# Performance work log

Hardware: AMD Instinct MI355X
Metric: run time of the kernel (lower is better)

## Reference

```python
import jax, jax.numpy as jnp
import numpy as np

B, T, D, H = 16, 2048, 1024, 64  # batch, seq_len(block_sz), emb_dim, head_sz


def setup_inputs() -> dict:
    key = jax.random.key(0)
    k0, k1, k2, k3 = jax.random.split(key, 4)
    x = jax.random.normal(k0, (B, T, D), dtype=jnp.float32)
    # nn.Linear(D, H, bias=False) weights, stored as [D, H] so y = x @ W
    s = 1.0 / np.sqrt(D)
    Wq = jax.random.uniform(k1, (D, H), dtype=jnp.float32, minval=-s, maxval=s)
    Wk = jax.random.uniform(k2, (D, H), dtype=jnp.float32, minval=-s, maxval=s)
    Wv = jax.random.uniform(k3, (D, H), dtype=jnp.float32, minval=-s, maxval=s)
    return {"x": x, "Wq": Wq, "Wk": Wk, "Wv": Wv}


def reference(x, Wq, Wk, Wv):
    # Single-head causal self-attention, naive (materializes full [B,T,T] scores).
    q = x @ Wq  # [B, T, H]
    k = x @ Wk  # [B, T, H]
    v = x @ Wv  # [B, T, H]
    scale = 1.0 / (q.shape[-1] ** 0.5)
    w = jnp.einsum("btd,bsd->bts", q, k) * scale  # [B, T, T]
    causal = jnp.tril(jnp.ones((T, T), dtype=bool))
    w = jnp.where(causal, w, -jnp.inf)
    w = jax.nn.softmax(w, axis=-1)
    # dropout p=0.0 -> identity
    out = jnp.einsum("bts,bsd->btd", w, v)  # [B, T, H]
    return out
```

## Files before the change

### kernel.cpp

```cpp
#include <hip/hip_runtime.h>
#include <hip/hip_bf16.h>
#include <math.h>

#define BB 16
#define TT 2048
#define DD 1024
#define HH 64
#define QK_SCALE 0.18033688011112042f

typedef short bf16x8 __attribute__((ext_vector_type(8)));
typedef short bf16x4 __attribute__((ext_vector_type(4)));
typedef float f32x4 __attribute__((ext_vector_type(4)));

__device__ __forceinline__ short f2bf(float f) {
  union { float f; unsigned u; } c; c.f = f;
  unsigned u = c.u + 0x7FFFu + ((c.u >> 16) & 1u);
  return (short)(u >> 16);
}

__device__ __forceinline__ unsigned pk2(float lo, float hi) {
  float2 t; t.x = lo; t.y = hi;
  __hip_bfloat162 h = __float22bfloat162_rn(t);
  union { __hip_bfloat162 h; unsigned u; } c; c.h = h;
  return c.u;
}

#define FENCE_VM(N)                                        \
  do {                                                     \
    asm volatile("s_waitcnt vmcnt(" #N ")" ::: "memory");  \
    __builtin_amdgcn_sched_barrier(0);                     \
    __builtin_amdgcn_s_barrier();                          \
  } while (0)

__device__ __forceinline__ void* lds_swz(void* base, int row, int col) {
  int byte = (row << 7) + (col << 1);
  byte ^= (row & 7) << 4;
  return (void*)((char*)base + byte);
}

__global__ __launch_bounds__(256) void pack_wt(
    const float* __restrict__ Wq, const float* __restrict__ Wk,
    const float* __restrict__ Wv, short* __restrict__ wt) {
  const int idx = blockIdx.x * 256 + threadIdx.x;
  const int n = idx >> 7;
  const int k0 = (idx & 127) << 3;
  const float* W = (n < 64) ? Wq : (n < 128) ? Wk : Wv;
  const int h = n & 63;
  bf16x8 o;
#pragma unroll
  for (int j = 0; j < 8; ++j) o[j] = f2bf(W[(k0 + j) * HH + h]);
  *(bf16x8*)&wt[n * DD + k0] = o;
}

__global__ __launch_bounds__(256, 2) void qkv_mfma(
    const float* __restrict__ x, const short* __restrict__ wt,
    short* __restrict__ qo, short* __restrict__ ko, short* __restrict__ vt) {
  __shared__ float xls[4][64 * 64];
  const int tid = threadIdx.x;
  const int lane = tid & 63;
  const int w = tid >> 6;
  const int q16 = lane & 15;
  const int g = lane >> 4;
  const size_t r0 = (size_t)blockIdx.x * 64;

  f32x4 acc[4][3];
#pragma unroll
  for (int mf = 0; mf < 4; ++mf)
#pragma unroll
    for (int nf = 0; nf < 3; ++nf) acc[mf][nf] = (f32x4){0.f, 0.f, 0.f, 0.f};

  const short* wp[3];
#pragma unroll
  for (int nf = 0; nf < 3; ++nf)
    wp[nf] = wt + (size_t)(w * 48 + nf * 16 + q16) * DD + g * 8;

  const int srow_b = w * 16 + (lane >> 4);
  const int ul = lane & 15;

  bf16x8 bcur[3][2];
#pragma unroll
  for (int nf = 0; nf < 3; ++nf)
#pragma unroll
    for (int kf = 0; kf < 2; ++kf)
      bcur[nf][kf] = *(const bf16x8*)(wp[nf] + kf * 32);
#pragma unroll
  for (int t = 0; t < 3; ++t)
#pragma unroll
    for (int j = 0; j < 4; ++j) {
      const int row = srow_b + j * 4;
      const int us = ul ^ (row & 15);
      const float* src = x + (r0 + row) * DD + t * 64 + us * 4;
      __builtin_amdgcn_global_load_lds(
          (const __attribute__((address_space(1))) void*)src,
          (__attribute__((address_space(3))) void*)(&xls[t][0] + (w * 4 + j) * 256),
          16, 0, 0);
    }
  __builtin_amdgcn_sched_barrier(0);
  FENCE_VM(8);

  for (int ks = 0; ks < 16; ++ks) {
    const float* bufc = &xls[ks & 3][0];

    bf16x8 bnxt[3][2];
    if (ks < 15) {
      const int k1 = (ks + 1) << 6;
#pragma unroll
      for (int nf = 0; nf < 3; ++nf)
#pragma unroll
        for (int kf = 0; kf < 2; ++kf)
          bnxt[nf][kf] = *(const bf16x8*)(wp[nf] + k1 + kf * 32);
    }
    if (ks <= 12) {
#pragma unroll
      for (int j = 0; j < 4; ++j) {
        const int row = srow_b + j * 4;
        const int us = ul ^ (row & 15);
        const float* src = x + (r0 + row) * DD + (ks + 3) * 64 + us * 4;
        __builtin_amdgcn_global_load_lds(
            (const __attribute__((address_space(1))) void*)src,
            (__attribute__((address_space(3))) void*)(&xls[(ks + 3) & 3][0] +
                                                      (w * 4 + j) * 256),
            16, 0, 0);
      }
    }
    __builtin_amdgcn_sched_barrier(0);

    bf16x8 afr[4][2];
#pragma unroll
    for (int mf = 0; mf < 4; ++mf)
#pragma unroll
      for (int kf = 0; kf < 2; ++kf) {
        const int R = mf * 16 + q16;
        const int r15 = R & 15;
        const int u0 = kf * 8 + g * 2;
        const float4 fa = *(const float4*)(bufc + R * 64 + ((u0 ^ r15) << 2));
        const float4 fb = *(const float4*)(bufc + R * 64 + (((u0 + 1) ^ r15) << 2));
        unsigned* up = (unsigned*)&afr[mf][kf];
        up[0] = pk2(fa.x, fa.y);
        up[1] = pk2(fa.z, fa.w);
        up[2] = pk2(fb.x, fb.y);
        up[3] = pk2(fb.z, fb.w);
      }

#pragma unroll
    for (int mf = 0; mf < 4; ++mf)
#pragma unroll
      for (int nf = 0; nf < 3; ++nf)
#pragma unroll
        for (int kf = 0; kf < 2; ++kf)
          acc[mf][nf] = __builtin_amdgcn_mfma_f32_16x16x32_bf16(
              afr[mf][kf], bcur[nf][kf], acc[mf][nf], 0, 0, 0);

    if (ks < 15) {
      if (ks <= 12) FENCE_VM(14);
      else if (ks == 13) FENCE_VM(10);
      else FENCE_VM(6);
#pragma unroll
      for (int nf = 0; nf < 3; ++nf)
#pragma unroll
        for (int kf = 0; kf < 2; ++kf) bcur[nf][kf] = bnxt[nf][kf];
    }
  }

#pragma unroll
  for (int nf = 0; nf < 3; ++nf) {
    const int n = w * 48 + nf * 16 + q16;
    const int mat = n >> 6;
    const int h = n & 63;
    if (mat < 2) {
      short* outp = mat ? ko : qo;
      const float fac = mat ? 1.0f : QK_SCALE;
#pragma unroll
      for (int mf = 0; mf < 4; ++mf)
#pragma unroll
        for (int r = 0; r < 4; ++r)
          outp[(r0 + mf * 16 + g * 4 + r) * HH + h] = f2bf(acc[mf][nf][r] * fac);
    } else {
      const int bb = (int)(r0 >> 11);
      const int tloc = (int)(r0 & 2047);
#pragma unroll
      for (int mf = 0; mf < 4; ++mf) {
        uint2 pkv;
        pkv.x = pk2(acc[mf][nf][0], acc[mf][nf][1]);
        pkv.y = pk2(acc[mf][nf][2], acc[mf][nf][3]);
        *(uint2*)&vt[((size_t)bb * HH + h) * TT + tloc + mf * 16 + g * 4] = pkv;
      }
    }
  }
}

__global__ __launch_bounds__(256, 4) void attn_mfma(
    const short* __restrict__ q, const short* __restrict__ k,
    const short* __restrict__ vt, float* __restrict__ out) {
  __shared__ short klds[2][64 * 64];
  __shared__ short vlds[2][64 * 64];

  const int id = blockIdx.x;
  const int b = (id & 7) | (((id >> 3) & 1) << 3);
  const int kk = id >> 4;
  const int qt = (kk < 16) ? (31 - kk) : (kk - 16);
  const int t0 = qt << 6;
  const int tid = threadIdx.x;
  const int lane = tid & 63;
  const int w = tid >> 6;
  const int q16 = lane & 15;
  const int g = lane >> 4;
  const int NC = qt + 1;

  const size_t brow = (size_t)b * TT;
  const short* kg = k + brow * HH;
  const short* vtg = vt + (size_t)b * HH * TT;

  const int srow = tid >> 2;
  const int scol = (tid & 3) << 4;

  const int vgA = (scol >> 3) & 3;
  const int vgB = ((scol + 8) >> 3) & 3;
  const int vm2 = scol >> 5;
  const short* vrow_p = vtg + srow * TT + vm2 * 32;

  bf16x8 kr0 = *(const bf16x8*)&kg[srow * HH + scol];
  bf16x8 kr1 = *(const bf16x8*)&kg[srow * HH + scol + 8];
  bf16x4 va0 = *(const bf16x4*)(vrow_p + 4 * vgA);
  bf16x4 va1 = *(const bf16x4*)(vrow_p + 16 + 4 * vgA);
  bf16x4 vb0 = *(const bf16x4*)(vrow_p + 4 * vgB);
  bf16x4 vb1 = *(const bf16x4*)(vrow_p + 16 + 4 * vgB);

  {
    const short* qsrc = q + (brow + t0 + srow) * HH;
    *(bf16x8*)lds_swz(klds[0], srow, scol) = *(const bf16x8*)&qsrc[scol];
    *(bf16x8*)lds_swz(klds[0], srow, scol + 8) = *(const bf16x8*)&qsrc[scol + 8];
  }
  __syncthreads();
  bf16x8 qa[2];
#pragma unroll
  for (int kf = 0; kf < 2; ++kf)
    qa[kf] = *(bf16x8*)lds_swz(klds[0], w * 16 + q16, kf * 32 + g * 8);
  __syncthreads();

  *(bf16x8*)lds_swz(klds[0], srow, scol) = kr0;
  *(bf16x8*)lds_swz(klds[0], srow, scol + 8) = kr1;
  *(bf16x8*)lds_swz(vlds[0], srow, scol) =
      __builtin_shufflevector(va0, va1, 0, 1, 2, 3, 4, 5, 6, 7);
  *(bf16x8*)lds_swz(vlds[0], srow, scol + 8) =
      __builtin_shufflevector(vb0, vb1, 0, 1, 2, 3, 4, 5, 6, 7);
  __syncthreads();

  f32x4 po[4];
  f32x4 lacc = (f32x4){0.f, 0.f, 0.f, 0.f};
  float m = -INFINITY;
#pragma unroll
  for (int nf = 0; nf < 4; ++nf) po[nf] = (f32x4){0.f, 0.f, 0.f, 0.f};

  const bf16x8 ones = {0x3F80, 0x3F80, 0x3F80, 0x3F80,
                       0x3F80, 0x3F80, 0x3F80, 0x3F80};
  int cur = 0;

  for (int c = 0; c < NC; ++c) {
    const bool notlast = (c + 1 < NC);
    if (notlast) {
      const int s1 = (c + 1) << 6;
      kr0 = *(const bf16x8*)&kg[(s1 + srow) * HH + scol];
      kr1 = *(const bf16x8*)&kg[(s1 + srow) * HH + scol + 8];
      va0 = *(const bf16x4*)(vrow_p + s1 + 4 * vgA);
      va1 = *(const bf16x4*)(vrow_p + s1 + 16 + 4 * vgA);
      vb0 = *(const bf16x4*)(vrow_p + s1 + 4 * vgB);
      vb1 = *(const bf16x4*)(vrow_p + s1 + 16 + 4 * vgB);
    }

    f32x4 sfr[4];
#pragma unroll
    for (int nf = 0; nf < 4; ++nf) sfr[nf] = (f32x4){0.f, 0.f, 0.f, 0.f};
    __builtin_amdgcn_s_setprio(1);
#pragma unroll
    for (int nf = 0; nf < 4; ++nf)
#pragma unroll
      for (int kf = 0; kf < 2; ++kf) {
        bf16x8 kb = *(bf16x8*)lds_swz(klds[cur], nf * 16 + q16, kf * 32 + g * 8);
        sfr[nf] = __builtin_amdgcn_mfma_f32_16x16x32_bf16(kb, qa[kf], sfr[nf], 0, 0, 0);
      }
    __builtin_amdgcn_s_setprio(0);

    if (c == NC - 1) {
      const int qloc = w * 16 + q16;
#pragma unroll
      for (int nf = 0; nf < 4; ++nf)
#pragma unroll
        for (int r = 0; r < 4; ++r)
          if (16 * nf + 4 * g + r > qloc) sfr[nf][r] = -INFINITY;
    }

    float pm;
    {
      f32x4 t01 = (f32x4){fmaxf(sfr[0][0], sfr[1][0]), fmaxf(sfr[0][1], sfr[1][1]),
                          fmaxf(sfr[0][2], sfr[1][2]), fmaxf(sfr[0][3], sfr[1][3])};
      f32x4 t23 = (f32x4){fmaxf(sfr[2][0], sfr[3][0]), fmaxf(sfr[2][1], sfr[3][1]),
                          fmaxf(sfr[2][2], sfr[3][2]), fmaxf(sfr[2][3], sfr[3][3])};
      pm = fmaxf(fmaxf(fmaxf(t01[0], t23[0]), fmaxf(t01[1], t23[1])),
                 fmaxf(fmaxf(t01[2], t23[2]), fmaxf(t01[3], t23[3])));
      pm = fmaxf(pm, __shfl_xor(pm, 16));
      pm = fmaxf(pm, __shfl_xor(pm, 32));
    }

    if (__any(pm - m > 8.f)) {
      const float mn = fmaxf(m, pm);
      const float corr = exp2f(m - mn);
      m = mn;
      const int sbase = (lane & 48) + ((lane >> 4) << 2);
#pragma unroll
      for (int r = 0; r < 4; ++r) {
        const float cr = __shfl(corr, sbase + r);
        lacc[r] *= cr;
#pragma unroll
        for (int nf = 0; nf < 4; ++nf) po[nf][r] *= cr;
      }
    }

    bf16x8 pa[2];
#pragma unroll
    for (int m2 = 0; m2 < 2; ++m2) {
      float e0 = exp2f(sfr[2 * m2][0] - m), e1 = exp2f(sfr[2 * m2][1] - m);
      float e2 = exp2f(sfr[2 * m2][2] - m), e3 = exp2f(sfr[2 * m2][3] - m);
      float e4 = exp2f(sfr[2 * m2 + 1][0] - m), e5 = exp2f(sfr[2 * m2 + 1][1] - m);
      float e6 = exp2f(sfr[2 * m2 + 1][2] - m), e7 = exp2f(sfr[2 * m2 + 1][3] - m);
      unsigned* up = (unsigned*)&pa[m2];
      up[0] = pk2(e0, e1); up[1] = pk2(e2, e3);
      up[2] = pk2(e4, e5); up[3] = pk2(e6, e7);
    }

    __builtin_amdgcn_s_setprio(1);
#pragma unroll
    for (int m2 = 0; m2 < 2; ++m2) {
#pragma unroll
      for (int nf = 0; nf < 4; ++nf) {
        bf16x8 vb = *(bf16x8*)lds_swz(vlds[cur], nf * 16 + q16, m2 * 32 + g * 8);
        po[nf] = __builtin_amdgcn_mfma_f32_16x16x32_bf16(pa[m2], vb, po[nf], 0, 0, 0);
      }
      lacc = __builtin_amdgcn_mfma_f32_16x16x32_bf16(pa[m2], ones, lacc, 0, 0, 0);
    }
    __builtin_amdgcn_s_setprio(0);

    if (notlast) {
      *(bf16x8*)lds_swz(klds[cur ^ 1], srow, scol) = kr0;
      *(bf16x8*)lds_swz(klds[cur ^ 1], srow, scol + 8) = kr1;
      *(bf16x8*)lds_swz(vlds[cur ^ 1], srow, scol) =
          __builtin_shufflevector(va0, va1, 0, 1, 2, 3, 4, 5, 6, 7);
      *(bf16x8*)lds_swz(vlds[cur ^ 1], srow, scol + 8) =
          __builtin_shufflevector(vb0, vb1, 0, 1, 2, 3, 4, 5, 6, 7);
      __syncthreads();
      cur ^= 1;
    }
  }

  const int qrow = t0 + w * 16 + g * 4;
#pragma unroll
  for (int nf = 0; nf < 4; ++nf) {
    const int h = nf * 16 + q16;
#pragma unroll
    for (int r = 0; r < 4; ++r)
      out[(brow + qrow + r) * HH + h] = po[nf][r] / lacc[r];
  }
}

extern "C" void kernel_launch(void* const* d_in, const int* in_sizes, int n_in,
                              void* d_out, int out_size, void* d_ws, size_t ws_size,
                              hipStream_t stream) {
  const float* x  = (const float*)d_in[0];
  const float* Wq = (const float*)d_in[1];
  const float* Wk = (const float*)d_in[2];
  const float* Wv = (const float*)d_in[3];
  float* out = (float*)d_out;

  const size_t bth = (size_t)BB * TT * HH;
  short* qb  = (short*)d_ws;
  short* kb  = qb + bth;
  short* vtb = kb + bth;
  short* wtb = vtb + bth;

  pack_wt<<<96, 256, 0, stream>>>(Wq, Wk, Wv, wtb);
  qkv_mfma<<<(BB * TT) / 64, 256, 0, stream>>>(x, wtb, qb, kb, vtb);
  attn_mfma<<<512, 256, 0, stream>>>(qb, kb, vtb, out);
}
```

Baseline: 78.55 us.

## Split long causal query tiles across two blocks and merge partials

Query tiles 16..31, which have the most key chunks, are now split into two halves of the KV range, each handled by its own block. Both halves write unnormalized partial outputs plus the running max and sum to workspace, and a new merge kernel rescales and combines them. This balances per-block work across 768 blocks and lowers the launch bound occupancy hint from 4 to 3. The cost is an extra kernel launch, global traffic for the partials, and extra workspace.

```diff
diff --git a/kernel.cpp b/kernel.cpp
--- a/kernel.cpp
+++ b/kernel.cpp
@@ -189,23 +189,30 @@
   }
 }
 
-__global__ __launch_bounds__(256, 4) void attn_mfma(
+__global__ __launch_bounds__(256, 3) void attn_mfma(
     const short* __restrict__ q, const short* __restrict__ k,
-    const short* __restrict__ vt, float* __restrict__ out) {
+    const short* __restrict__ vt, float* __restrict__ out,
+    float* __restrict__ po0f, float* __restrict__ mlf) {
   __shared__ short klds[2][64 * 64];
   __shared__ short vlds[2][64 * 64];
 
   const int id = blockIdx.x;
   const int b = (id & 7) | (((id >> 3) & 1) << 3);
-  const int kk = id >> 4;
-  const int qt = (kk < 16) ? (31 - kk) : (kk - 16);
+  const int wc = id >> 4;
+  int qt, c0, c1, mode;
+  if (wc < 16) {
+    qt = 31 - wc; mode = 1; c0 = 0; c1 = (qt + 2) >> 1;
+  } else if (wc < 32) {
+    qt = 31 - (wc - 16); mode = 2; c0 = (qt + 2) >> 1; c1 = qt + 1;
+  } else {
+    qt = 47 - wc; mode = 0; c0 = 0; c1 = qt + 1;
+  }
   const int t0 = qt << 6;
   const int tid = threadIdx.x;
   const int lane = tid & 63;
   const int w = tid >> 6;
   const int q16 = lane & 15;
   const int g = lane >> 4;
-  const int NC = qt + 1;
 
   const size_t brow = (size_t)b * TT;
   const short* kg = k + brow * HH;
@@ -219,12 +226,13 @@
   const int vm2 = scol >> 5;
   const short* vrow_p = vtg + srow * TT + vm2 * 32;
 
-  bf16x8 kr0 = *(const bf16x8*)&kg[srow * HH + scol];
-  bf16x8 kr1 = *(const bf16x8*)&kg[srow * HH + scol + 8];
-  bf16x4 va0 = *(const bf16x4*)(vrow_p + 4 * vgA);
-  bf16x4 va1 = *(const bf16x4*)(vrow_p + 16 + 4 * vgA);
-  bf16x4 vb0 = *(const bf16x4*)(vrow_p + 4 * vgB);
-  bf16x4 vb1 = *(const bf16x4*)(vrow_p + 16 + 4 * vgB);
+  const int s00 = c0 << 6;
+  bf16x8 kr0 = *(const bf16x8*)&kg[(s00 + srow) * HH + scol];
+  bf16x8 kr1 = *(const bf16x8*)&kg[(s00 + srow) * HH + scol + 8];
+  bf16x4 va0 = *(const bf16x4*)(vrow_p + s00 + 4 * vgA);
+  bf16x4 va1 = *(const bf16x4*)(vrow_p + s00 + 16 + 4 * vgA);
+  bf16x4 vb0 = *(const bf16x4*)(vrow_p + s00 + 4 * vgB);
+  bf16x4 vb1 = *(const bf16x4*)(vrow_p + s00 + 16 + 4 * vgB);
 
   {
     const short* qsrc = q + (brow + t0 + srow) * HH;
@@ -256,8 +264,8 @@
                        0x3F80, 0x3F80, 0x3F80, 0x3F80};
   int cur = 0;
 
-  for (int c = 0; c < NC; ++c) {
-    const bool notlast = (c + 1 < NC);
+  for (int c = c0; c < c1; ++c) {
+    const bool notlast = (c + 1 < c1);
     if (notlast) {
       const int s1 = (c + 1) << 6;
       kr0 = *(const bf16x8*)&kg[(s1 + srow) * HH + scol];
@@ -281,7 +289,7 @@
       }
     __builtin_amdgcn_s_setprio(0);
 
-    if (c == NC - 1) {
+    if (mode != 1 && c == c1 - 1) {
       const int qloc = w * 16 + q16;
 #pragma unroll
       for (int nf = 0; nf < 4; ++nf)
@@ -352,14 +360,56 @@
     }
   }
 
-  const int qrow = t0 + w * 16 + g * 4;
-#pragma unroll
-  for (int nf = 0; nf < 4; ++nf) {
-    const int h = nf * 16 + q16;
-#pragma unroll
-    for (int r = 0; r < 4; ++r)
-      out[(brow + qrow + r) * HH + h] = po[nf][r] / lacc[r];
-  }
+  if (mode == 0) {
+    const int qrow = t0 + w * 16 + g * 4;
+#pragma unroll
+    for (int nf = 0; nf < 4; ++nf) {
+      const int h = nf * 16 + q16;
+#pragma unroll
+      for (int r = 0; r < 4; ++r)
+        out[(brow + qrow + r) * HH + h] = po[nf][r] / lacc[r];
+    }
+  } else {
+    float* dst = (mode == 1) ? (po0f + (size_t)((b << 4) + qt - 16) * 4096)
+                             : (out + (brow + t0) * HH);
+#pragma unroll
+    for (int nf = 0; nf < 4; ++nf) {
+      const int h = nf * 16 + q16;
+#pragma unroll
+      for (int r = 0; r < 4; ++r)
+        dst[(w * 16 + 4 * g + r) * HH + h] = po[nf][r];
+    }
+    const int mlbase = ((b << 4) + qt - 16) * 64;
+    float* mArr = mlf + ((mode == 1) ? 0 : 32768);
+    float* lArr = mlf + ((mode == 1) ? 16384 : 49152);
+    if (g == 0) mArr[mlbase + w * 16 + q16] = m;
+    if (q16 == 0) {
+#pragma unroll
+      for (int r = 0; r < 4; ++r) lArr[mlbase + w * 16 + 4 * g + r] = lacc[r];
+    }
+  }
+}
+
+__global__ __launch_bounds__(256) void attn_merge(
+    const float* __restrict__ po0f, const float* __restrict__ mlf,
+    float* __restrict__ out) {
+  const int idx = blockIdx.x * 256 + threadIdx.x;
+  const int bt = idx >> 12;
+  const int qh = idx & 4095;
+  const int qq = qh >> 6;
+  const int b = bt >> 4;
+  const int qt = (bt & 15) + 16;
+  const float m0 = mlf[bt * 64 + qq];
+  const float l0 = mlf[16384 + bt * 64 + qq];
+  const float m1 = mlf[32768 + bt * 64 + qq];
+  const float l1 = mlf[49152 + bt * 64 + qq];
+  const float p0 = po0f[idx];
+  const size_t oidx = ((size_t)b * TT + (qt << 6) + qq) * HH + (qh & 63);
+  const float p1 = out[oidx];
+  const float ms = fmaxf(m0, m1);
+  const float e0 = exp2f(m0 - ms);
+  const float e1 = exp2f(m1 - ms);
+  out[oidx] = (p0 * e0 + p1 * e1) / (l0 * e0 + l1 * e1);
 }
 
 extern "C" void kernel_launch(void* const* d_in, const int* in_sizes, int n_in,
@@ -376,8 +426,11 @@
   short* kb  = qb + bth;
   short* vtb = kb + bth;
   short* wtb = vtb + bth;
+  float* po0f = (float*)(wtb + 192 * 1024);
+  float* mlf  = po0f + (size_t)1048576;
 
   pack_wt<<<96, 256, 0, stream>>>(Wq, Wk, Wv, wtb);
   qkv_mfma<<<(BB * TT) / 64, 256, 0, stream>>>(x, wtb, qb, kb, vtb);
-  attn_mfma<<<512, 256, 0, stream>>>(qb, kb, vtb, out);
-}
+  attn_mfma<<<768, 256, 0, stream>>>(qb, kb, vtb, out, po0f, mlf);
+  attn_merge<<<4096, 256, 0, stream>>>(po0f, mlf, out);
+}
```

New measurement: 78.33 us. About the same (-0.3%).
